# Kernel tuning notes

Hardware: AMD Instinct MI355X
Metric: run time of the kernel (lower is better)

## Reference

```python
import jax, jax.numpy as jnp
import numpy as np

FEATS = [(100, 100), (50, 50), (25, 25), (13, 13)]  # (W, H) per level
BS, NQ, D = 2, 10000, 256
NH, NL, NP, G = 8, 4, 4, 8
HD = D // NH


def grid_sample_bilinear(im, grid):
    """torch.nn.functional.grid_sample(mode='bilinear', padding_mode='zeros', align_corners=False).
    im: [N, C, H, W]; grid: [N, Hg, Wg, 2] in [-1, 1] (x, y). Returns [N, C, Hg, Wg]."""
    N, C, H, W = im.shape
    Hg, Wg = grid.shape[1], grid.shape[2]
    x = (grid[..., 0] + 1.0) * (W * 0.5) - 0.5
    y = (grid[..., 1] + 1.0) * (H * 0.5) - 0.5
    x0 = jnp.floor(x); y0 = jnp.floor(y)
    wx1 = x - x0; wx0 = 1.0 - wx1
    wy1 = y - y0; wy0 = 1.0 - wy1
    imf = im.reshape(N, C, H * W)

    def corner(xi, yi, w):
        inb = (xi >= 0) & (xi < W) & (yi >= 0) & (yi < H)
        xi_c = jnp.clip(xi, 0, W - 1).astype(jnp.int32)
        yi_c = jnp.clip(yi, 0, H - 1).astype(jnp.int32)
        idx = (yi_c * W + xi_c).reshape(N, 1, Hg * Wg)
        vals = jnp.take_along_axis(imf, idx, axis=2).reshape(N, C, Hg, Wg)
        return vals * (w * inb.astype(im.dtype))[:, None]

    out = (corner(x0, y0, wx0 * wy0) + corner(x0 + 1, y0, wx1 * wy0)
           + corner(x0, y0 + 1, wx0 * wy1) + corner(x0 + 1, y0 + 1, wx1 * wy1))
    return out


def setup_inputs() -> dict:
    key = jax.random.key(0)
    ks = jax.random.split(key, 7)
    nv = sum(w * h for (w, h) in FEATS)
    return {
        "query": jax.random.normal(ks[0], (BS, NQ, D), jnp.float32),
        "value": jax.random.normal(ks[1], (BS, nv, NH, HD), jnp.float32),
        "reference_points": jax.random.uniform(ks[2], (BS, NQ, NL, 2), jnp.float32),
        "spatial_shapes": jnp.array(FEATS, jnp.float32),  # rows are (W, H)
        "W_off": jax.random.normal(ks[3], (NH * NL * NP * 2, D), jnp.float32) * 0.02,
        "b_off": jax.random.normal(ks[4], (NH * NL * NP * 2,), jnp.float32) * 0.5,
        "W_attn": jax.random.normal(ks[5], (NH * NL * NP, D), jnp.float32) * 0.02,
        "b_attn": jax.random.normal(ks[6], (NH * NL * NP,), jnp.float32) * 0.02,
    }


def reference(query, value, reference_points, spatial_shapes, W_off, b_off, W_attn, b_attn):
    bs, nq, _ = query.shape
    # sampling offsets: [bs, nq, NH, NL*NP*2] with (level, point, xy) layout
    off = (jnp.einsum('bqd,od->bqo', query, W_off) + b_off).reshape(bs, nq, NH, NL * NP * 2)
    # reference points tiled to the same (level, point, xy) layout
    ref = jnp.broadcast_to(reference_points[:, :, None, :, None, :],
                           (bs, nq, NH, NL, NP, 2)).reshape(bs, nq, NH, NL * NP * 2)
    # offset normalizer: (1/W, 1/H) per level, tiled over points
    inv = 1.0 / spatial_shapes  # [NL, 2]
    norm = jnp.broadcast_to(inv[:, None, :], (NL, NP, 2)).reshape(-1)
    loc = (ref + off * norm) * 2.0 - 1.0  # [bs, nq, NH, NL*NP*2]
    loc = loc.reshape(bs, nq, NH, NL, NP, 2)

    # attention weights: softmax over (NL*NP), then rearranged to [bs*NH, 1, nq/G, NL*G*NP]
    aw = jax.nn.softmax((jnp.einsum('bqd,od->bqo', query, W_attn) + b_attn)
                        .reshape(bs, nq, NH, NL * NP), axis=-1)
    aw = aw.reshape(bs, nq // G, G, NH, NL, NP).transpose(0, 3, 1, 4, 2, 5)
    aw = aw.reshape(bs * NH, 1, nq // G, NL * G * NP)

    # per-level grid_sample
    sizes = [w * h for (w, h) in FEATS]
    starts = np.concatenate([[0], np.cumsum(sizes)]).tolist()
    sampled = []
    for lvl, (Wl, Hl) in enumerate(FEATS):
        val_l = value[:, starts[lvl]:starts[lvl + 1]]  # [bs, Hl*Wl, NH, HD]
        val_l = val_l.transpose(0, 2, 3, 1).reshape(bs * NH, HD, Hl, Wl)
        grid_l = loc[:, :, :, lvl].transpose(0, 2, 1, 3, 4)  # [bs, NH, nq, NP, 2]
        grid_l = grid_l.reshape(bs * NH, nq // G, G * NP, 2)
        sampled.append(grid_sample_bilinear(val_l, grid_l))  # [bs*NH, HD, nq/G, G*NP]
    sv = jnp.concatenate(sampled, axis=-1)  # [bs*NH, HD, nq/G, NL*G*NP]

    out = sv * aw
    # reduce_sum linear (fixed 0/1 weight from init_weights) == sum over levels and points per group slot
    out = out.reshape(bs * NH, HD, nq // G, NL, G, NP).sum(axis=(3, 5))  # [bs*NH, HD, nq/G, G]
    return out.reshape(bs, NH * HD, nq)
```

## Files before the change

kernel.cpp:

```cpp
#include <hip/hip_runtime.h>

#define NQ   10000
#define BSZ  2
#define DIM  256
#define NH   8
#define HD   32
#define NLV  4
#define NPT  4
#define NV   13294
#define MT   (BSZ*NQ)
#define NOUT 384

typedef float  floatx4 __attribute__((ext_vector_type(4)));
typedef int    intx4   __attribute__((ext_vector_type(4)));
typedef __bf16 bf16x8  __attribute__((ext_vector_type(8)));

__device__ __forceinline__ unsigned short f32_to_bf16(float f) {
  unsigned int u = __float_as_uint(f);
  u += 0x7FFFu + ((u >> 16) & 1u);
  return (unsigned short)(u >> 16);
}

__global__ __launch_bounds__(256) void cast_kernel(
    const float* __restrict__ query, const float* __restrict__ W_off,
    const float* __restrict__ W_attn,
    unsigned short* __restrict__ Qb, unsigned short* __restrict__ Wb) {
  int i = blockIdx.x * 256 + threadIdx.x;
  if (i < 5120000) {
    Qb[i] = f32_to_bf16(query[i]);
  } else if (i < 5218304) {
    int j = i - 5120000;
    float v = (j < 65536) ? W_off[j] : W_attn[j - 65536];
    Wb[j] = f32_to_bf16(v);
  }
}

__global__ __launch_bounds__(256) void gemm_kernel(
    const unsigned short* __restrict__ Qb, const unsigned short* __restrict__ Wb,
    const float* __restrict__ b_off, const float* __restrict__ b_attn,
    float* __restrict__ raw) {
  __shared__ unsigned short As[64][40];
  __shared__ unsigned short Bs[64][40];
  const int m0 = blockIdx.x * 64;
  const int n0 = blockIdx.y * 64;
  const int tid  = threadIdx.x;
  const int wave = tid >> 6;
  const int lane = tid & 63;
  const int quad = lane >> 4;
  const int l16  = lane & 15;
  floatx4 acc[4] = {{0.f,0.f,0.f,0.f},{0.f,0.f,0.f,0.f},
                    {0.f,0.f,0.f,0.f},{0.f,0.f,0.f,0.f}};
  const int ar = tid >> 2;
  const int ac = (tid & 3) * 8;

  for (int k0 = 0; k0 < DIM; k0 += 32) {
    int gm = m0 + ar;
    uint4 av = make_uint4(0u,0u,0u,0u);
    if (gm < MT) av = *(const uint4*)&Qb[gm*DIM + k0 + ac];
    uint4 bv = *(const uint4*)&Wb[(n0 + ar)*DIM + k0 + ac];
    *(uint4*)&As[ar][ac] = av;
    *(uint4*)&Bs[ar][ac] = bv;
    __syncthreads();
    bf16x8 a = *(const bf16x8*)&As[wave*16 + l16][quad*8];
    #pragma unroll
    for (int nt = 0; nt < 4; nt++) {
      bf16x8 b = *(const bf16x8*)&Bs[nt*16 + l16][quad*8];
      acc[nt] = __builtin_amdgcn_mfma_f32_16x16x32_bf16(a, b, acc[nt], 0, 0, 0);
    }
    __syncthreads();
  }
  #pragma unroll
  for (int nt = 0; nt < 4; nt++) {
    int gn = n0 + nt*16 + l16;
    float bias = (gn < 256) ? b_off[gn] : b_attn[gn - 256];
    #pragma unroll
    for (int r = 0; r < 4; r++) {
      int gm = m0 + wave*16 + quad*4 + r;
      if (gm < MT) raw[gm*NOUT + gn] = acc[nt][r] + bias;
    }
  }
}

__global__ __launch_bounds__(256) void sample_kernel(
    const float* __restrict__ raw, const float* __restrict__ value,
    const float* __restrict__ refp, float* __restrict__ tmp) {
  const int b  = blockIdx.y;
  const int q0 = blockIdx.x * 4;
  const int mbase = b * NQ + q0;
  const int tid = threadIdx.x;

  __shared__ float s_px[512], s_py[512], s_logit[512];
  __shared__ int   s_tab[4 * 8 * 132];

  const int WLI[4] = {100, 50, 25, 13};
  const int STI[4] = {0, 10000, 12500, 13125};

  #pragma unroll
  for (int it = 0; it < 2; ++it) {
    int slot = it * 256 + tid;
    int ql = slot >> 7, r = slot & 127, h = r >> 4, lp = r & 15, l = lp >> 2, p = lp & 3;
    int m = mbase + ql;
    const float* rp = raw + m * NOUT;
    float offx = rp[h*32 + l*8 + p*2 + 0];
    float offy = rp[h*32 + l*8 + p*2 + 1];
    s_logit[slot] = rp[256 + h*16 + lp];
    float Wl = (float)WLI[l];
    float rx = refp[(m*NLV + l)*2 + 0];
    float ry = refp[(m*NLV + l)*2 + 1];
    s_px[slot] = rx * Wl + offx - 0.5f;
    s_py[slot] = ry * Wl + offy - 0.5f;
  }
  __syncthreads();

  if (tid < 32) {
    int base = tid * 16;
    float mx = -1e30f;
    #pragma unroll
    for (int i = 0; i < 16; i++) mx = fmaxf(mx, s_logit[base + i]);
    float s = 0.f;
    float e[16];
    #pragma unroll
    for (int i = 0; i < 16; i++) { e[i] = expf(s_logit[base + i] - mx); s += e[i]; }
    float inv = 1.f / s;
    #pragma unroll
    for (int i = 0; i < 16; i++) s_logit[base + i] = e[i] * inv;
  }
  __syncthreads();

  #pragma unroll
  for (int it = 0; it < 2; ++it) {
    int slot = it * 256 + tid;
    int ql = slot >> 7, r = slot & 127, h = r >> 4, lp = r & 15, l = lp >> 2;
    float px = s_px[slot], py = s_py[slot], aw = s_logit[slot];
    float x0f = floorf(px), y0f = floorf(py);
    int x0 = (int)x0f, y0 = (int)y0f;
    float wx1 = px - x0f, wx0 = 1.f - wx1;
    float wy1 = py - y0f, wy0 = 1.f - wy1;
    int Wl = WLI[l], STl = STI[l];
    int row = (ql*8 + h) * 132 + lp * 8;
    #pragma unroll
    for (int t = 0; t < 4; ++t) {
      int xi = x0 + (t & 1), yi = y0 + (t >> 1);
      bool inb = (xi >= 0) & (xi < Wl) & (yi >= 0) & (yi < Wl);
      int off = inb ? ((STl + yi*Wl + xi) * 1024 + h * 128) : 0;
      float w = inb ? (aw * ((t & 1) ? wx1 : wx0) * ((t >> 1) ? wy1 : wy0)) : 0.f;
      s_tab[row + t]     = off;
      s_tab[row + 4 + t] = __float_as_int(w);
    }
  }
  __syncthreads();

  const int ql = tid >> 6, lane = tid & 63, h = lane >> 3, cq = lane & 7;
  const char* vb = (const char*)value + (size_t)b * (NV*NH*HD*4) + cq * 16;
  floatx4 acc = {0.f, 0.f, 0.f, 0.f};
  const int rbase = (ql*8 + h) * 132;
  #pragma unroll 4
  for (int pt = 0; pt < 16; ++pt) {
    intx4   offs = *(const intx4*)  &s_tab[rbase + pt*8];
    floatx4 ws   = *(const floatx4*)&s_tab[rbase + pt*8 + 4];
    floatx4 v0 = *(const floatx4*)(vb + offs.x);
    floatx4 v1 = *(const floatx4*)(vb + offs.y);
    floatx4 v2 = *(const floatx4*)(vb + offs.z);
    floatx4 v3 = *(const floatx4*)(vb + offs.w);
    acc += ws.x * v0;
    acc += ws.y * v1;
    acc += ws.z * v2;
    acc += ws.w * v3;
  }
  int m = mbase + ql;
  *(floatx4*)&tmp[(size_t)m * DIM + h*HD + cq*4] = acc;
}

__global__ __launch_bounds__(256) void transpose_kernel(
    const float* __restrict__ tmp, float* __restrict__ out) {
  __shared__ float tile[32][33];
  const int b  = blockIdx.z;
  const int q0 = blockIdx.x * 32;
  const int c0 = blockIdx.y * 32;
  const int tx = threadIdx.x & 31;
  const int ty = threadIdx.x >> 5;
  #pragma unroll
  for (int i = 0; i < 4; i++) {
    int qq = q0 + ty + i*8;
    tile[ty + i*8][tx] = (qq < NQ) ? tmp[((long)b*NQ + qq)*DIM + c0 + tx] : 0.f;
  }
  __syncthreads();
  if (q0 + tx < NQ) {
    #pragma unroll
    for (int i = 0; i < 4; i++) {
      out[((long)b*DIM + c0 + ty + i*8)*NQ + q0 + tx] = tile[tx][ty + i*8];
    }
  }
}

extern "C" void kernel_launch(void* const* d_in, const int* in_sizes, int n_in,
                              void* d_out, int out_size, void* d_ws, size_t ws_size,
                              hipStream_t stream) {
  const float* query  = (const float*)d_in[0];
  const float* value  = (const float*)d_in[1];
  const float* refp   = (const float*)d_in[2];
  const float* W_off  = (const float*)d_in[4];
  const float* b_off  = (const float*)d_in[5];
  const float* W_attn = (const float*)d_in[6];
  const float* b_attn = (const float*)d_in[7];
  float* out = (float*)d_out;

  char* ws = (char*)d_ws;
  unsigned short* Qb  = (unsigned short*)ws;
  float*          tmp = (float*)ws;
  unsigned short* Wb  = (unsigned short*)(ws + 20480000);
  float*          raw = (float*)(ws + 20480000 + 196608);

  hipLaunchKernelGGL(cast_kernel, dim3((5218304 + 255) / 256), dim3(256), 0, stream,
                     query, W_off, W_attn, Qb, Wb);
  hipLaunchKernelGGL(gemm_kernel, dim3(313, 6), dim3(256), 0, stream,
                     Qb, Wb, b_off, b_attn, raw);
  hipLaunchKernelGGL(sample_kernel, dim3(NQ / 4, BSZ), dim3(256), 0, stream,
                     raw, value, refp, tmp);
  hipLaunchKernelGGL(transpose_kernel, dim3(313, 8, 2), dim3(256), 0, stream,
                     tmp, out);
}
```

Measured before the change: 183.2 us.

## Fuse bf16 cast into GEMM and output transpose into sampling kernel

Removes the separate cast kernel by converting fp32 query and weights to bf16 while loading GEMM tiles. The GEMM tile widens to 128 columns, and the grid is reordered so column blocks are adjacent. The final transpose kernel is dropped: the sampling kernel stages its results in shared memory (aliased with the earlier buffers) and writes the transposed output directly. This cuts two launches and the round trips of the bf16 copy and the intermediate tmp buffer. In exchange, output stores are now only 16 bytes per channel row per block, and the GEMM does more conversion work per load.

After: 187.4 us. +2.3%, slower.

```diff
diff --git a/kernel.cpp b/kernel.cpp
--- a/kernel.cpp
+++ b/kernel.cpp
@@ -21,76 +21,90 @@
   return (unsigned short)(u >> 16);
 }
 
-__global__ __launch_bounds__(256) void cast_kernel(
+__global__ __launch_bounds__(256) void gemm_kernel(
     const float* __restrict__ query, const float* __restrict__ W_off,
     const float* __restrict__ W_attn,
-    unsigned short* __restrict__ Qb, unsigned short* __restrict__ Wb) {
-  int i = blockIdx.x * 256 + threadIdx.x;
-  if (i < 5120000) {
-    Qb[i] = f32_to_bf16(query[i]);
-  } else if (i < 5218304) {
-    int j = i - 5120000;
-    float v = (j < 65536) ? W_off[j] : W_attn[j - 65536];
-    Wb[j] = f32_to_bf16(v);
-  }
-}
-
-__global__ __launch_bounds__(256) void gemm_kernel(
-    const unsigned short* __restrict__ Qb, const unsigned short* __restrict__ Wb,
     const float* __restrict__ b_off, const float* __restrict__ b_attn,
     float* __restrict__ raw) {
   __shared__ unsigned short As[64][40];
-  __shared__ unsigned short Bs[64][40];
-  const int m0 = blockIdx.x * 64;
-  const int n0 = blockIdx.y * 64;
+  __shared__ unsigned short Bs[128][40];
+  const int n0 = blockIdx.x * 128;
+  const int m0 = blockIdx.y * 64;
   const int tid  = threadIdx.x;
   const int wave = tid >> 6;
   const int lane = tid & 63;
   const int quad = lane >> 4;
   const int l16  = lane & 15;
-  floatx4 acc[4] = {{0.f,0.f,0.f,0.f},{0.f,0.f,0.f,0.f},
-                    {0.f,0.f,0.f,0.f},{0.f,0.f,0.f,0.f}};
+  floatx4 acc[8] = {};
   const int ar = tid >> 2;
   const int ac = (tid & 3) * 8;
+  const int br = tid >> 1;
+  const int bc = (tid & 1) * 16;
+  const float* __restrict__ Wsrc =
+      (n0 < 256) ? (W_off + (size_t)n0 * DIM) : (W_attn + (size_t)(n0 - 256) * DIM);
 
   for (int k0 = 0; k0 < DIM; k0 += 32) {
-    int gm = m0 + ar;
-    uint4 av = make_uint4(0u,0u,0u,0u);
-    if (gm < MT) av = *(const uint4*)&Qb[gm*DIM + k0 + ac];
-    uint4 bv = *(const uint4*)&Wb[(n0 + ar)*DIM + k0 + ac];
-    *(uint4*)&As[ar][ac] = av;
-    *(uint4*)&Bs[ar][ac] = bv;
+    {
+      int gm = m0 + ar;
+      floatx4 a0 = {}, a1 = {};
+      if (gm < MT) {
+        const float* src = query + (size_t)gm * DIM + k0 + ac;
+        a0 = *(const floatx4*)src;
+        a1 = *(const floatx4*)(src + 4);
+      }
+      unsigned short t[8];
+      t[0]=f32_to_bf16(a0.x); t[1]=f32_to_bf16(a0.y); t[2]=f32_to_bf16(a0.z); t[3]=f32_to_bf16(a0.w);
+      t[4]=f32_to_bf16(a1.x); t[5]=f32_to_bf16(a1.y); t[6]=f32_to_bf16(a1.z); t[7]=f32_to_bf16(a1.w);
+      *(uint4*)&As[ar][ac] = *(const uint4*)t;
+    }
+    {
+      const float* src = Wsrc + (size_t)br * DIM + k0 + bc;
+      floatx4 b0 = *(const floatx4*)src;
+      floatx4 b1 = *(const floatx4*)(src + 4);
+      floatx4 b2 = *(const floatx4*)(src + 8);
+      floatx4 b3 = *(const floatx4*)(src + 12);
+      unsigned short t[16];
+      t[0]=f32_to_bf16(b0.x);  t[1]=f32_to_bf16(b0.y);  t[2]=f32_to_bf16(b0.z);  t[3]=f32_to_bf16(b0.w);
+      t[4]=f32_to_bf16(b1.x);  t[5]=f32_to_bf16(b1.y);  t[6]=f32_to_bf16(b1.z);  t[7]=f32_to_bf16(b1.w);
+      t[8]=f32_to_bf16(b2.x);  t[9]=f32_to_bf16(b2.y);  t[10]=f32_to_bf16(b2.z); t[11]=f32_to_bf16(b2.w);
+      t[12]=f32_to_bf16(b3.x); t[13]=f32_to_bf16(b3.y); t[14]=f32_to_bf16(b3.z); t[15]=f32_to_bf16(b3.w);
+      *(uint4*)&Bs[br][bc]     = *(const uint4*)t;
+      *(uint4*)&Bs[br][bc + 8] = *(const uint4*)(t + 8);
+    }
     __syncthreads();
     bf16x8 a = *(const bf16x8*)&As[wave*16 + l16][quad*8];
     #pragma unroll
-    for (int nt = 0; nt < 4; nt++) {
+    for (int nt = 0; nt < 8; nt++) {
       bf16x8 b = *(const bf16x8*)&Bs[nt*16 + l16][quad*8];
       acc[nt] = __builtin_amdgcn_mfma_f32_16x16x32_bf16(a, b, acc[nt], 0, 0, 0);
     }
     __syncthreads();
   }
   #pragma unroll
-  for (int nt = 0; nt < 4; nt++) {
+  for (int nt = 0; nt < 8; nt++) {
     int gn = n0 + nt*16 + l16;
     float bias = (gn < 256) ? b_off[gn] : b_attn[gn - 256];
     #pragma unroll
     for (int r = 0; r < 4; r++) {
       int gm = m0 + wave*16 + quad*4 + r;
-      if (gm < MT) raw[gm*NOUT + gn] = acc[nt][r] + bias;
+      if (gm < MT) raw[(size_t)gm*NOUT + gn] = acc[nt][r] + bias;
     }
   }
 }
 
 __global__ __launch_bounds__(256) void sample_kernel(
     const float* __restrict__ raw, const float* __restrict__ value,
-    const float* __restrict__ refp, float* __restrict__ tmp) {
+    const float* __restrict__ refp, float* __restrict__ out) {
   const int b  = blockIdx.y;
   const int q0 = blockIdx.x * 4;
   const int mbase = b * NQ + q0;
   const int tid = threadIdx.x;
 
-  __shared__ float s_px[512], s_py[512], s_logit[512];
-  __shared__ int   s_tab[4 * 8 * 132];
+  __shared__ union {
+    struct { float px[512]; float py[512]; float logit[512]; } a;
+    float outbuf[1120];
+  } u;
+  __shared__ int s_tab[4 * 8 * 132];
 
   const int WLI[4] = {100, 50, 25, 13};
   const int STI[4] = {0, 10000, 12500, 13125};
@@ -100,15 +114,15 @@
     int slot = it * 256 + tid;
     int ql = slot >> 7, r = slot & 127, h = r >> 4, lp = r & 15, l = lp >> 2, p = lp & 3;
     int m = mbase + ql;
-    const float* rp = raw + m * NOUT;
+    const float* rp = raw + (size_t)m * NOUT;
     float offx = rp[h*32 + l*8 + p*2 + 0];
     float offy = rp[h*32 + l*8 + p*2 + 1];
-    s_logit[slot] = rp[256 + h*16 + lp];
+    u.a.logit[slot] = rp[256 + h*16 + lp];
     float Wl = (float)WLI[l];
     float rx = refp[(m*NLV + l)*2 + 0];
     float ry = refp[(m*NLV + l)*2 + 1];
-    s_px[slot] = rx * Wl + offx - 0.5f;
-    s_py[slot] = ry * Wl + offy - 0.5f;
+    u.a.px[slot] = rx * Wl + offx - 0.5f;
+    u.a.py[slot] = ry * Wl + offy - 0.5f;
   }
   __syncthreads();
 
@@ -116,14 +130,14 @@
     int base = tid * 16;
     float mx = -1e30f;
     #pragma unroll
-    for (int i = 0; i < 16; i++) mx = fmaxf(mx, s_logit[base + i]);
+    for (int i = 0; i < 16; i++) mx = fmaxf(mx, u.a.logit[base + i]);
     float s = 0.f;
     float e[16];
     #pragma unroll
-    for (int i = 0; i < 16; i++) { e[i] = expf(s_logit[base + i] - mx); s += e[i]; }
+    for (int i = 0; i < 16; i++) { e[i] = expf(u.a.logit[base + i] - mx); s += e[i]; }
     float inv = 1.f / s;
     #pragma unroll
-    for (int i = 0; i < 16; i++) s_logit[base + i] = e[i] * inv;
+    for (int i = 0; i < 16; i++) u.a.logit[base + i] = e[i] * inv;
   }
   __syncthreads();
 
@@ -131,7 +145,7 @@
   for (int it = 0; it < 2; ++it) {
     int slot = it * 256 + tid;
     int ql = slot >> 7, r = slot & 127, h = r >> 4, lp = r & 15, l = lp >> 2;
-    float px = s_px[slot], py = s_py[slot], aw = s_logit[slot];
+    float px = u.a.px[slot], py = u.a.py[slot], aw = u.a.logit[slot];
     float x0f = floorf(px), y0f = floorf(py);
     int x0 = (int)x0f, y0 = (int)y0f;
     float wx1 = px - x0f, wx0 = 1.f - wx1;
@@ -150,46 +164,40 @@
   }
   __syncthreads();
 
-  const int ql = tid >> 6, lane = tid & 63, h = lane >> 3, cq = lane & 7;
-  const char* vb = (const char*)value + (size_t)b * (NV*NH*HD*4) + cq * 16;
-  floatx4 acc = {0.f, 0.f, 0.f, 0.f};
-  const int rbase = (ql*8 + h) * 132;
-  #pragma unroll 4
-  for (int pt = 0; pt < 16; ++pt) {
-    intx4   offs = *(const intx4*)  &s_tab[rbase + pt*8];
-    floatx4 ws   = *(const floatx4*)&s_tab[rbase + pt*8 + 4];
-    floatx4 v0 = *(const floatx4*)(vb + offs.x);
-    floatx4 v1 = *(const floatx4*)(vb + offs.y);
-    floatx4 v2 = *(const floatx4*)(vb + offs.z);
-    floatx4 v3 = *(const floatx4*)(vb + offs.w);
-    acc += ws.x * v0;
-    acc += ws.y * v1;
-    acc += ws.z * v2;
-    acc += ws.w * v3;
-  }
-  int m = mbase + ql;
-  *(floatx4*)&tmp[(size_t)m * DIM + h*HD + cq*4] = acc;
-}
-
-__global__ __launch_bounds__(256) void transpose_kernel(
-    const float* __restrict__ tmp, float* __restrict__ out) {
-  __shared__ float tile[32][33];
-  const int b  = blockIdx.z;
-  const int q0 = blockIdx.x * 32;
-  const int c0 = blockIdx.y * 32;
-  const int tx = threadIdx.x & 31;
-  const int ty = threadIdx.x >> 5;
-  #pragma unroll
-  for (int i = 0; i < 4; i++) {
-    int qq = q0 + ty + i*8;
-    tile[ty + i*8][tx] = (qq < NQ) ? tmp[((long)b*NQ + qq)*DIM + c0 + tx] : 0.f;
-  }
-  __syncthreads();
-  if (q0 + tx < NQ) {
-    #pragma unroll
-    for (int i = 0; i < 4; i++) {
-      out[((long)b*DIM + c0 + ty + i*8)*NQ + q0 + tx] = tile[tx][ty + i*8];
-    }
+  {
+    const int ql = tid >> 6, lane = tid & 63, h = lane >> 3, cq = lane & 7;
+    const char* vb = (const char*)value + (size_t)b * (NV*NH*HD*4) + cq * 16;
+    floatx4 acc = {0.f, 0.f, 0.f, 0.f};
+    const int rbase = (ql*8 + h) * 132;
+    #pragma unroll 4
+    for (int pt = 0; pt < 16; ++pt) {
+      intx4   offs = *(const intx4*)  &s_tab[rbase + pt*8];
+      floatx4 ws   = *(const floatx4*)&s_tab[rbase + pt*8 + 4];
+      floatx4 v0 = *(const floatx4*)(vb + offs.x);
+      floatx4 v1 = *(const floatx4*)(vb + offs.y);
+      floatx4 v2 = *(const floatx4*)(vb + offs.z);
+      floatx4 v3 = *(const floatx4*)(vb + offs.w);
+      acc += ws.x * v0;
+      acc += ws.y * v1;
+      acc += ws.z * v2;
+      acc += ws.w * v3;
+    }
+    int obase = ql*280 + h*33 + cq*4;
+    u.outbuf[obase + 0] = acc.x;
+    u.outbuf[obase + 1] = acc.y;
+    u.outbuf[obase + 2] = acc.z;
+    u.outbuf[obase + 3] = acc.w;
+  }
+  __syncthreads();
+
+  {
+    const int ch = tid, h = ch >> 5, c = ch & 31;
+    floatx4 o;
+    o.x = u.outbuf[0*280 + h*33 + c];
+    o.y = u.outbuf[1*280 + h*33 + c];
+    o.z = u.outbuf[2*280 + h*33 + c];
+    o.w = u.outbuf[3*280 + h*33 + c];
+    *(floatx4*)&out[((size_t)(b*DIM + ch))*NQ + q0] = o;
   }
 }
 
@@ -205,18 +213,10 @@
   const float* b_attn = (const float*)d_in[7];
   float* out = (float*)d_out;
 
-  char* ws = (char*)d_ws;
-  unsigned short* Qb  = (unsigned short*)ws;
-  float*          tmp = (float*)ws;
-  unsigned short* Wb  = (unsigned short*)(ws + 20480000);
-  float*          raw = (float*)(ws + 20480000 + 196608);
-
-  hipLaunchKernelGGL(cast_kernel, dim3((5218304 + 255) / 256), dim3(256), 0, stream,
-                     query, W_off, W_attn, Qb, Wb);
-  hipLaunchKernelGGL(gemm_kernel, dim3(313, 6), dim3(256), 0, stream,
-                     Qb, Wb, b_off, b_attn, raw);
+  float* raw = (float*)d_ws;
+
+  hipLaunchKernelGGL(gemm_kernel, dim3(3, 313), dim3(256), 0, stream,
+                     query, W_off, W_attn, b_off, b_attn, raw);
   hipLaunchKernelGGL(sample_kernel, dim3(NQ / 4, BSZ), dim3(256), 0, stream,
-                     raw, value, refp, tmp);
-  hipLaunchKernelGGL(transpose_kernel, dim3(313, 8, 2), dim3(256), 0, stream,
-                     tmp, out);
-}
+                     raw, value, refp, out);
+}
```
